# Performance work log

Hardware: AMD Instinct MI355X
Metric: run time of the kernel (lower is better)

Reference implementation:

```python
import jax, jax.numpy as jnp
import numpy as np
from jax import lax

NMS_SIZE = 5
THR = 0.0
B, C, H, W = 8, 1, 2048, 2048
# fixed capacity for the jit-compatible nonzero (padded with -1); generous upper
# bound on number of surviving local maxima (~HW/25 per map, half above thr=0)
MAX_KEYPOINTS = 2_000_000


def setup_inputs() -> dict:
    key = jax.random.key(0)
    scores = jax.random.normal(key, (B, C, H, W), dtype=jnp.float32)
    return {"scores": scores}


def _local_max(scores):
    # MaxPool2d(kernel=5, stride=1, padding=2) == SAME-padded windowed max
    return lax.reduce_window(
        scores,
        -jnp.inf,
        lax.max,
        window_dimensions=(1, 1, NMS_SIZE, NMS_SIZE),
        window_strides=(1, 1, 1, 1),
        padding="SAME",
    )


def reference(scores):
    maxima = (scores == _local_max(scores)) & (scores > THR)  # [B,C,H,W] bool
    # torch: maxima.nonzero().t()[2:4] -> (row, col) coordinates of survivors.
    # jit-compatible fixed-size nonzero, padded with -1 (extra entries beyond
    # the true count are fill values, matching a compacted index list).
    _, _, hh, ww = jnp.nonzero(maxima, size=MAX_KEYPOINTS, fill_value=-1)
    return jnp.stack([hh, ww])  # [2, MAX_KEYPOINTS] int
```

## Files before the change

### kernel.cpp

```cpp
#include <hip/hip_runtime.h>
#include <stdint.h>
#include <math.h>

#define BATCH 8
#define HH 2048
#define WW 2048
#define R 16
#define NSTRIPS (HH / R)
#define NBLK (NSTRIPS * BATCH)
#define BLK_WORDS (R * WW / 32)
#define MAXK 2000000
#define FILLB 1024
#define OUT_I4 ((2 * MAXK) / 4)

__global__ __launch_bounds__(256) void nms_mask_fill(const float* __restrict__ scores,
                                                     uint8_t* __restrict__ maskbytes,
                                                     int* __restrict__ counts,
                                                     int* __restrict__ out) {
    const int tid  = threadIdx.x;

    if (blockIdx.x >= NBLK) {
        const int fb = (int)blockIdx.x - NBLK;
        const int4 neg = make_int4(-1, -1, -1, -1);
        int4* o = (int4*)out;
        for (int i = fb * 256 + tid; i < OUT_I4; i += FILLB * 256)
            o[i] = neg;
        return;
    }

    const int chunk = blockIdx.x;
    const int b     = chunk >> 7;
    const int strip = chunk & (NSTRIPS - 1);
    const int h0    = strip * R;
    const int lane  = tid & 63;
    const int wv    = tid >> 6;
    const int c0    = wv * 512 + lane * 8;
    const float* colp = scores + (size_t)b * HH * WW + c0;
    const bool has_l = (c0 != 0);
    const bool has_r = (c0 != WW - 8);

    float win[5][12];

#define LOAD_ROW(PH, hrow)                                                    \
    do {                                                                      \
        const int h_ = (hrow);                                                \
        if ((unsigned)h_ < (unsigned)HH) {                                    \
            const float* p_ = colp + (size_t)h_ * WW;                         \
            float4 a_ = *(const float4*)(p_);                                 \
            float4 b_ = *(const float4*)(p_ + 4);                             \
            win[PH][2] = a_.x; win[PH][3] = a_.y;                             \
            win[PH][4] = a_.z; win[PH][5] = a_.w;                             \
            win[PH][6] = b_.x; win[PH][7] = b_.y;                             \
            win[PH][8] = b_.z; win[PH][9] = b_.w;                             \
            if (has_l) {                                                      \
                float2 hl_ = *(const float2*)(p_ - 2);                        \
                win[PH][0] = hl_.x; win[PH][1] = hl_.y;                       \
            } else { win[PH][0] = -INFINITY; win[PH][1] = -INFINITY; }        \
            if (has_r) {                                                      \
                float2 hr_ = *(const float2*)(p_ + 8);                        \
                win[PH][10] = hr_.x; win[PH][11] = hr_.y;                     \
            } else { win[PH][10] = -INFINITY; win[PH][11] = -INFINITY; }      \
        } else {                                                              \
            _Pragma("unroll")                                                 \
            for (int k_ = 0; k_ < 12; ++k_) win[PH][k_] = -INFINITY;          \
        }                                                                     \
    } while (0)

    LOAD_ROW(0, h0 - 2);
    LOAD_ROW(1, h0 - 1);
    LOAD_ROW(2, h0 + 0);
    LOAD_ROW(3, h0 + 1);

    int pc = 0;
    size_t outbyte = (((size_t)(b * HH + h0) * WW) + c0) >> 3;

#pragma unroll
    for (int i = 0; i < R; ++i) {
        LOAD_ROW((4 + i) % 5, h0 + 2 + i);
        const int CEN = (2 + i) % 5;

        float v[12];
#pragma unroll
        for (int k = 0; k < 12; ++k)
            v[k] = fmaxf(fmaxf(fmaxf(win[0][k], win[1][k]),
                               fmaxf(win[2][k], win[3][k])), win[4][k]);
        float p[11];
#pragma unroll
        for (int k = 0; k < 11; ++k) p[k] = fmaxf(v[k], v[k + 1]);

        uint32_t byte = 0;
#pragma unroll
        for (int j = 0; j < 8; ++j) {
            const float hm = fmaxf(fmaxf(p[j], p[j + 2]), v[j + 4]);
            const float s  = win[CEN][j + 2];
            if ((s == hm) && (s > 0.0f)) byte |= (1u << j);
        }
        maskbytes[outbyte] = (uint8_t)byte;
        outbyte += WW / 8;
        pc += __popc(byte);
    }
#undef LOAD_ROW

#pragma unroll
    for (int d = 32; d >= 1; d >>= 1) pc += __shfl_down(pc, d, 64);
    __shared__ int wsum[4];
    if (lane == 0) wsum[wv] = pc;
    __syncthreads();
    if (tid == 0) counts[chunk] = wsum[0] + wsum[1] + wsum[2] + wsum[3];
}

__global__ __launch_bounds__(256) void compact(const uint32_t* __restrict__ bitmask,
                                               const int* __restrict__ counts,
                                               int* __restrict__ out_h,
                                               int* __restrict__ out_w) {
    const int chunk = blockIdx.x;
    const int tid   = threadIdx.x;
    const int lane  = tid & 63, wv = tid >> 6;

    const uint4 c4 = ((const uint4*)counts)[tid];
    const int i0 = tid * 4;
    int contrib = 0;
    contrib += (i0 + 0 < chunk) ? (int)c4.x : 0;
    contrib += (i0 + 1 < chunk) ? (int)c4.y : 0;
    contrib += (i0 + 2 < chunk) ? (int)c4.z : 0;
    contrib += (i0 + 3 < chunk) ? (int)c4.w : 0;

    int red = contrib;
#pragma unroll
    for (int d = 32; d >= 1; d >>= 1) red += __shfl_down(red, d, 64);
    __shared__ int ws[4];
    __shared__ int base_s;
    if (lane == 0) ws[wv] = red;
    __syncthreads();
    if (tid == 0) base_s = ws[0] + ws[1] + ws[2] + ws[3];

    const uint32_t* mbase = bitmask + (size_t)chunk * BLK_WORDS;
    const uint4 m = ((const uint4*)mbase)[tid];
    const int pc = __popc(m.x) + __popc(m.y) + __popc(m.z) + __popc(m.w);

    int incl = pc;
#pragma unroll
    for (int d = 1; d < 64; d <<= 1) {
        int n = __shfl_up(incl, d, 64);
        if (lane >= d) incl += n;
    }
    __shared__ int wsums[4];
    if (lane == 63) wsums[wv] = incl;
    __syncthreads();
    int wbase = 0;
    for (int i = 0; i < wv; ++i) wbase += wsums[i];

    const int h0 = (chunk & (NSTRIPS - 1)) * R;
    int off = base_s + wbase + (incl - pc);

    uint32_t words[4] = {m.x, m.y, m.z, m.w};
    const uint32_t local0 = (uint32_t)tid * 128u;
#pragma unroll
    for (int wj = 0; wj < 4; ++wj) {
        uint32_t mm = words[wj];
        const uint32_t lb = local0 + (uint32_t)wj * 32u;
        while (mm) {
            const int bit = __ffs(mm) - 1;
            mm &= mm - 1;
            const uint32_t L = lb + (uint32_t)bit;
            if (off < MAXK) {
                out_h[off] = h0 + (int)(L >> 11);
                out_w[off] = (int)(L & 2047u);
            }
            ++off;
        }
    }
}

extern "C" void kernel_launch(void* const* d_in, const int* in_sizes, int n_in,
                              void* d_out, int out_size, void* d_ws, size_t ws_size,
                              hipStream_t stream) {
    const float* scores = (const float*)d_in[0];
    int* out = (int*)d_out;

    uint32_t* bitmask = (uint32_t*)d_ws;
    int* counts = (int*)((char*)d_ws + (size_t)NBLK * BLK_WORDS * 4);

    nms_mask_fill<<<NBLK + FILLB, 256, 0, stream>>>(scores, (uint8_t*)bitmask,
                                                    counts, out);
    compact<<<NBLK, 256, 0, stream>>>(bitmask, counts, out, out + MAXK);
}
```

Before: 43.14 us.

## Move -1 tail fill into compact, halve strip height, swizzle block order

The -1 padding of the output is no longer written by extra blocks in the mask kernel. Instead the compact kernel computes the total survivor count and fills only the entries past that total, which avoids writing the whole 16 MB output twice. Strip height drops from 16 to 8 rows, which doubles the block count but raises halo reread overhead. Mask blocks are also remapped so that consecutive block IDs are spread across batches.

```diff
diff --git a/kernel.cpp b/kernel.cpp
--- a/kernel.cpp
+++ b/kernel.cpp
@@ -5,35 +5,25 @@
 #define BATCH 8
 #define HH 2048
 #define WW 2048
-#define R 16
+#define R 8
 #define NSTRIPS (HH / R)
 #define NBLK (NSTRIPS * BATCH)
 #define BLK_WORDS (R * WW / 32)
 #define MAXK 2000000
-#define FILLB 1024
-#define OUT_I4 ((2 * MAXK) / 4)
-
-__global__ __launch_bounds__(256) void nms_mask_fill(const float* __restrict__ scores,
-                                                     uint8_t* __restrict__ maskbytes,
-                                                     int* __restrict__ counts,
-                                                     int* __restrict__ out) {
+#define TAIL_I4 (MAXK / 4)
+#define TAIL_PER_BLK ((TAIL_I4 + NBLK - 1) / NBLK)
+
+__global__ __launch_bounds__(256) void nms_mask(const float* __restrict__ scores,
+                                                uint8_t* __restrict__ maskbytes,
+                                                int* __restrict__ counts) {
+    const int chunk = (int)(blockIdx.x % 8) * (NBLK / 8) + (int)(blockIdx.x / 8);
+
     const int tid  = threadIdx.x;
-
-    if (blockIdx.x >= NBLK) {
-        const int fb = (int)blockIdx.x - NBLK;
-        const int4 neg = make_int4(-1, -1, -1, -1);
-        int4* o = (int4*)out;
-        for (int i = fb * 256 + tid; i < OUT_I4; i += FILLB * 256)
-            o[i] = neg;
-        return;
-    }
-
-    const int chunk = blockIdx.x;
-    const int b     = chunk >> 7;
+    const int lane = tid & 63;
+    const int wv   = tid >> 6;
+    const int b     = chunk >> 8;
     const int strip = chunk & (NSTRIPS - 1);
     const int h0    = strip * R;
-    const int lane  = tid & 63;
-    const int wv    = tid >> 6;
     const int c0    = wv * 512 + lane * 8;
     const float* colp = scores + (size_t)b * HH * WW + c0;
     const bool has_l = (c0 != 0);
@@ -113,30 +103,34 @@
                                                const int* __restrict__ counts,
                                                int* __restrict__ out_h,
                                                int* __restrict__ out_w) {
-    const int chunk = blockIdx.x;
+    const int chunk = (int)blockIdx.x;
     const int tid   = threadIdx.x;
     const int lane  = tid & 63, wv = tid >> 6;
 
-    const uint4 c4 = ((const uint4*)counts)[tid];
-    const int i0 = tid * 4;
-    int contrib = 0;
-    contrib += (i0 + 0 < chunk) ? (int)c4.x : 0;
-    contrib += (i0 + 1 < chunk) ? (int)c4.y : 0;
-    contrib += (i0 + 2 < chunk) ? (int)c4.z : 0;
-    contrib += (i0 + 3 < chunk) ? (int)c4.w : 0;
-
-    int red = contrib;
-#pragma unroll
-    for (int d = 32; d >= 1; d >>= 1) red += __shfl_down(red, d, 64);
-    __shared__ int ws[4];
-    __shared__ int base_s;
-    if (lane == 0) ws[wv] = red;
-    __syncthreads();
-    if (tid == 0) base_s = ws[0] + ws[1] + ws[2] + ws[3];
-
-    const uint32_t* mbase = bitmask + (size_t)chunk * BLK_WORDS;
-    const uint4 m = ((const uint4*)mbase)[tid];
-    const int pc = __popc(m.x) + __popc(m.y) + __popc(m.z) + __popc(m.w);
+    const uint4 ca = ((const uint4*)counts)[2 * tid];
+    const uint4 cb = ((const uint4*)counts)[2 * tid + 1];
+    const int i0 = tid * 8;
+    int contrib = 0, full = 0;
+    {
+        const uint32_t cv[8] = {ca.x, ca.y, ca.z, ca.w, cb.x, cb.y, cb.z, cb.w};
+#pragma unroll
+        for (int j = 0; j < 8; ++j) {
+            full += (int)cv[j];
+            contrib += (i0 + j < chunk) ? (int)cv[j] : 0;
+        }
+    }
+
+    int rA = contrib, rB = full;
+#pragma unroll
+    for (int d = 32; d >= 1; d >>= 1) {
+        rA += __shfl_down(rA, d, 64);
+        rB += __shfl_down(rB, d, 64);
+    }
+    __shared__ int wsA[4], wsB[4], wscan[4];
+    if (lane == 0) { wsA[wv] = rA; wsB[wv] = rB; }
+
+    const uint2 m = ((const uint2*)(bitmask + (size_t)chunk * BLK_WORDS))[tid];
+    const int pc = __popc(m.x) + __popc(m.y);
 
     int incl = pc;
 #pragma unroll
@@ -144,19 +138,22 @@
         int n = __shfl_up(incl, d, 64);
         if (lane >= d) incl += n;
     }
-    __shared__ int wsums[4];
-    if (lane == 63) wsums[wv] = incl;
+    if (lane == 63) wscan[wv] = incl;
     __syncthreads();
+
+    const int chunk_base = wsA[0] + wsA[1] + wsA[2] + wsA[3];
+    int total = wsB[0] + wsB[1] + wsB[2] + wsB[3];
+    if (total > MAXK) total = MAXK;
     int wbase = 0;
-    for (int i = 0; i < wv; ++i) wbase += wsums[i];
+    for (int i = 0; i < wv; ++i) wbase += wscan[i];
 
     const int h0 = (chunk & (NSTRIPS - 1)) * R;
-    int off = base_s + wbase + (incl - pc);
-
-    uint32_t words[4] = {m.x, m.y, m.z, m.w};
-    const uint32_t local0 = (uint32_t)tid * 128u;
-#pragma unroll
-    for (int wj = 0; wj < 4; ++wj) {
+    int off = chunk_base + wbase + (incl - pc);
+
+    uint32_t words[2] = {m.x, m.y};
+    const uint32_t local0 = (uint32_t)tid * 64u;
+#pragma unroll
+    for (int wj = 0; wj < 2; ++wj) {
         uint32_t mm = words[wj];
         const uint32_t lb = local0 + (uint32_t)wj * 32u;
         while (mm) {
@@ -170,6 +167,25 @@
             ++off;
         }
     }
+
+    const int i4base = chunk * TAIL_PER_BLK;
+    for (int t = tid; t < TAIL_PER_BLK; t += 256) {
+        const int i4 = i4base + t;
+        if (i4 >= TAIL_I4) break;
+        const int base = i4 * 4;
+        if (base + 4 <= total) continue;
+        if (base >= total) {
+            const int4 neg = make_int4(-1, -1, -1, -1);
+            *(int4*)(out_h + base) = neg;
+            *(int4*)(out_w + base) = neg;
+        } else {
+#pragma unroll
+            for (int j = 0; j < 4; ++j) {
+                const int idx = base + j;
+                if (idx >= total) { out_h[idx] = -1; out_w[idx] = -1; }
+            }
+        }
+    }
 }
 
 extern "C" void kernel_launch(void* const* d_in, const int* in_sizes, int n_in,
@@ -181,7 +197,6 @@
     uint32_t* bitmask = (uint32_t*)d_ws;
     int* counts = (int*)((char*)d_ws + (size_t)NBLK * BLK_WORDS * 4);
 
-    nms_mask_fill<<<NBLK + FILLB, 256, 0, stream>>>(scores, (uint8_t*)bitmask,
-                                                    counts, out);
+    nms_mask<<<NBLK, 256, 0, stream>>>(scores, (uint8_t*)bitmask, counts);
     compact<<<NBLK, 256, 0, stream>>>(bitmask, counts, out, out + MAXK);
 }
```

After: 46.00 us. 6.6% more time.
